# Optimization experiments

Hardware: AMD Instinct MI355X
Metric: run time of the kernel (lower is better)

## Reference

```python
import jax, jax.numpy as jnp
import numpy as np

QI8 = 127.0      # qint8 symmetric max
QI16 = 32767.0   # qint16 symmetric max
MIN_SUB_OUT = -12.0  # SegmentLUT exp input_range lower bound
EPS = 1e-9


def _fq(x, scale, qmax):
    # fake-quantize with straight-through estimator
    q = jnp.clip(jnp.round(x / scale), -qmax - 1.0, qmax) * scale
    return x + jax.lax.stop_gradient(q - x)


def _fq_auto(x, qmax):
    # symmetric max-abs observer (scale is not differentiated, as in QAT)
    s = jax.lax.stop_gradient(jnp.maximum(jnp.max(jnp.abs(x)), EPS)) / qmax
    return _fq(x, s, qmax)


def setup_inputs() -> dict:
    key = jax.random.key(0)
    # pre-softmax logits, quantized with scale 0.0625 -> int8 range ~[-8, 8]
    x = jax.random.normal(key, (8, 4096, 1024), dtype=jnp.float32) * 2.0
    scale = jnp.ones((1,), dtype=jnp.float32) * 0.0625
    return {"x": x, "scale": scale}


def reference(x, scale):
    dim = 1
    # input fake-quant to qint8 grid with given scale (QuantiSoftmaxFunction.forward)
    xq = _fq(x, scale, QI8)
    # sub: x - max(x, dim), qint16 fake-quant (FloatFunctional.sub with int16 qconfig)
    sub = xq - jnp.max(xq, axis=dim, keepdims=True)  # values in (-inf, 0]
    # SegmentLUT exp: input clipped to [min_sub_out, 0], zero gradient below range
    sub = _fq_auto(jnp.clip(sub, MIN_SUB_OUT, 0.0), QI16)
    e = _fq_auto(jnp.exp(sub), QI16)               # LUT exp, qint16 out
    s = _fq_auto(jnp.sum(e, axis=dim, keepdims=True), QI16)  # qint16 sum
    r = _fq_auto(1.0 / s, QI16)                    # LUT reciprocal, qint16
    out = _fq_auto(e * r, QI8)                     # final mul, qint8 output
    return out
```

## Files before the change

kernel.cpp:

```cpp
#include <hip/hip_runtime.h>
#include <math.h>


typedef float       f4 __attribute__((ext_vector_type(4)));
typedef signed char c4 __attribute__((ext_vector_type(4)));

static constexpr int Bdim = 8;
static constexpr int Jdim = 4096;
static constexpr int Cdim = 1024;
static constexpr int JCHUNK = 16;
static constexpr int NJC = Jdim / JCHUNK;
static constexpr int NG = Bdim * Cdim;
static constexpr int PSIZE = Bdim * NJC * Cdim;

static constexpr int SC_OFF   = 0;
static constexpr int GMAX_OFF = 16;
static constexpr int S_OFF    = GMAX_OFF + NG;
static constexpr int PS_OFF   = S_OFF + NG;
static constexpr size_t FB_FLOATS   = (size_t)PS_OFF + PSIZE;
static constexpr size_t FB_BYTES    = FB_FLOATS * 4;
static constexpr size_t CODES_BYTES = (size_t)Bdim * Jdim * Cdim;
static constexpr size_t P_BYTES     = 2 * (size_t)PSIZE;

__device__ __forceinline__ float code8(float x, float sinv) {
    return fminf(fmaxf(rintf(x * sinv), -128.0f), 127.0f);
}

__device__ __forceinline__ float eq_from(float xq, float gmv, float ssub_inv, float ssub) {
    float sub = fminf(fmaxf(xq - gmv, -12.0f), 0.0f);
    float q   = rintf(sub * ssub_inv);
    float e   = __expf(q * ssub);
    return rintf(e * 32767.0f) * (1.0f / 32767.0f);
}

template <bool WC>
__global__ __launch_bounds__(256) void k_pass1(const float* __restrict__ x,
                                               const float* __restrict__ scale,
                                               float* __restrict__ fbuf,
                                               signed char* __restrict__ codes,
                                               signed char* __restrict__ pmax,
                                               signed char* __restrict__ pmin) {
    if (blockIdx.x == 0 && threadIdx.x == 0) {
        fbuf[SC_OFF + 0] = 0.0f;
        fbuf[SC_OFF + 1] = 0.0f;
        fbuf[SC_OFF + 2] = __int_as_float(0x7f800000);
    }
    const int b  = blockIdx.x / NJC;
    const int jc = blockIdx.x % NJC;
    const int c0 = threadIdx.x * 4;
    const float sinv = 1.0f / scale[0];
    const size_t base = ((size_t)(b * Jdim + jc * JCHUNK)) * Cdim + c0;

    f4 vmax = {-1e30f, -1e30f, -1e30f, -1e30f};
    f4 vmin = { 1e30f,  1e30f,  1e30f,  1e30f};
    #pragma unroll 4
    for (int r = 0; r < JCHUNK; ++r) {
        const f4 v = __builtin_nontemporal_load(
            reinterpret_cast<const f4*>(x + base + (size_t)r * Cdim));
        f4 q;
        q[0] = code8(v[0], sinv); q[1] = code8(v[1], sinv);
        q[2] = code8(v[2], sinv); q[3] = code8(v[3], sinv);
        vmax[0] = fmaxf(vmax[0], q[0]); vmin[0] = fminf(vmin[0], q[0]);
        vmax[1] = fmaxf(vmax[1], q[1]); vmin[1] = fminf(vmin[1], q[1]);
        vmax[2] = fmaxf(vmax[2], q[2]); vmin[2] = fminf(vmin[2], q[2]);
        vmax[3] = fmaxf(vmax[3], q[3]); vmin[3] = fminf(vmin[3], q[3]);
        if (WC) {
            c4 pk = {(signed char)(int)q[0], (signed char)(int)q[1],
                     (signed char)(int)q[2], (signed char)(int)q[3]};
            *reinterpret_cast<c4*>(codes + base + (size_t)r * Cdim) = pk;
        }
    }
    const size_t pidx = ((size_t)(b * NJC + jc)) * Cdim + c0;
    c4 mx = {(signed char)(int)vmax[0], (signed char)(int)vmax[1],
             (signed char)(int)vmax[2], (signed char)(int)vmax[3]};
    c4 mn = {(signed char)(int)vmin[0], (signed char)(int)vmin[1],
             (signed char)(int)vmin[2], (signed char)(int)vmin[3]};
    *reinterpret_cast<c4*>(pmax + pidx) = mx;
    *reinterpret_cast<c4*>(pmin + pidx) = mn;
}

__global__ __launch_bounds__(256) void k_reduce1(const float* __restrict__ scale,
                                                 float* __restrict__ fbuf,
                                                 const signed char* __restrict__ pmax,
                                                 const signed char* __restrict__ pmin) {
    const int b   = blockIdx.x / 32;
    const int ct  = blockIdx.x % 32;
    const int ci  = threadIdx.x & 31;
    const int sub = threadIdx.x >> 5;
    const int c   = ct * 32 + ci;

    int mx = -128, mn = 127;
    for (int jc = sub; jc < NJC; jc += 8) {
        const size_t idx = ((size_t)(b * NJC + jc)) * Cdim + c;
        mx = max(mx, (int)pmax[idx]);
        mn = min(mn, (int)pmin[idx]);
    }
    __shared__ int smx[8][32], smn[8][32];
    smx[sub][ci] = mx; smn[sub][ci] = mn;
    __syncthreads();
    for (int off = 4; off; off >>= 1) {
        if (sub < off) {
            smx[sub][ci] = max(smx[sub][ci], smx[sub + off][ci]);
            smn[sub][ci] = min(smn[sub][ci], smn[sub + off][ci]);
        }
        __syncthreads();
    }
    __shared__ float sd[32];
    if (sub == 0) {
        const float s = scale[0];
        const float gmaxv = (float)smx[0][ci] * s;
        const float gminv = (float)smn[0][ci] * s;
        fbuf[GMAX_OFF + b * Cdim + c] = (float)smx[0][ci];
        sd[ci] = fminf(12.0f, gmaxv - gminv);
    }
    __syncthreads();
    if (threadIdx.x == 0) {
        float m = sd[0];
        #pragma unroll
        for (int i = 1; i < 32; ++i) m = fmaxf(m, sd[i]);
        atomicMax(reinterpret_cast<unsigned int*>(fbuf + SC_OFF + 0), __float_as_uint(m));
    }
}

template <bool UC>
__global__ __launch_bounds__(256) void k_pass2(const float* __restrict__ x,
                                               const signed char* __restrict__ codes,
                                               const float* __restrict__ scale,
                                               float* __restrict__ fbuf) {
    const int b  = blockIdx.x / NJC;
    const int jc = blockIdx.x % NJC;
    const int c0 = threadIdx.x * 4;
    const float s = scale[0];
    const float sinv = 1.0f / s;
    const float amax = fmaxf(fbuf[SC_OFF + 0], 1e-9f);
    const float ssub = amax / 32767.0f;
    const float ssub_inv = 1.0f / ssub;
    const f4 gmc = *reinterpret_cast<const f4*>(fbuf + GMAX_OFF + b * Cdim + c0);
    const float gm0 = gmc[0] * s, gm1 = gmc[1] * s, gm2 = gmc[2] * s, gm3 = gmc[3] * s;
    const size_t base = ((size_t)(b * Jdim + jc * JCHUNK)) * Cdim + c0;

    float a0 = 0.f, a1 = 0.f, a2 = 0.f, a3 = 0.f;
    #pragma unroll 4
    for (int r = 0; r < JCHUNK; ++r) {
        float xq0, xq1, xq2, xq3;
        if (UC) {
            const c4 q = *reinterpret_cast<const c4*>(codes + base + (size_t)r * Cdim);
            xq0 = (float)q[0] * s; xq1 = (float)q[1] * s;
            xq2 = (float)q[2] * s; xq3 = (float)q[3] * s;
        } else {
            const f4 v = *reinterpret_cast<const f4*>(x + base + (size_t)r * Cdim);
            xq0 = code8(v[0], sinv) * s; xq1 = code8(v[1], sinv) * s;
            xq2 = code8(v[2], sinv) * s; xq3 = code8(v[3], sinv) * s;
        }
        a0 += eq_from(xq0, gm0, ssub_inv, ssub);
        a1 += eq_from(xq1, gm1, ssub_inv, ssub);
        a2 += eq_from(xq2, gm2, ssub_inv, ssub);
        a3 += eq_from(xq3, gm3, ssub_inv, ssub);
    }
    f4 acc = {a0, a1, a2, a3};
    *reinterpret_cast<f4*>(fbuf + PS_OFF + ((size_t)(b * NJC + jc)) * Cdim + c0) = acc;
}

__global__ __launch_bounds__(256) void k_reduce2(float* __restrict__ fbuf) {
    const int b   = blockIdx.x / 32;
    const int ct  = blockIdx.x % 32;
    const int ci  = threadIdx.x & 31;
    const int sub = threadIdx.x >> 5;
    const int c   = ct * 32 + ci;

    float p = 0.0f;
    for (int jc = sub; jc < NJC; jc += 8)
        p += fbuf[PS_OFF + ((size_t)(b * NJC + jc)) * Cdim + c];
    __shared__ float sp[8][32];
    sp[sub][ci] = p;
    __syncthreads();
    for (int off = 4; off; off >>= 1) {
        if (sub < off) sp[sub][ci] += sp[sub + off][ci];
        __syncthreads();
    }
    __shared__ float smx[32], smn[32];
    if (sub == 0) {
        const float t = sp[0][ci];
        fbuf[S_OFF + b * Cdim + c] = t;
        smx[ci] = t; smn[ci] = t;
    }
    __syncthreads();
    if (threadIdx.x == 0) {
        float mx = smx[0], mn = smn[0];
        #pragma unroll
        for (int i = 1; i < 32; ++i) { mx = fmaxf(mx, smx[i]); mn = fminf(mn, smn[i]); }
        atomicMax(reinterpret_cast<unsigned int*>(fbuf + SC_OFF + 1), __float_as_uint(mx));
        atomicMin(reinterpret_cast<unsigned int*>(fbuf + SC_OFF + 2), __float_as_uint(mn));
    }
}

template <bool UC>
__global__ __launch_bounds__(256) void k_pass3(const float* __restrict__ x,
                                               const signed char* __restrict__ codes,
                                               const float* __restrict__ scale,
                                               const float* __restrict__ fbuf,
                                               float* __restrict__ out) {
    const int b  = blockIdx.x / NJC;
    const int jc = blockIdx.x % NJC;
    const int c0 = threadIdx.x * 4;
    const float s = scale[0];
    const float sinv = 1.0f / s;

    const float amax = fmaxf(fbuf[SC_OFF + 0], 1e-9f);
    const float ssub = amax / 32767.0f;
    const float ssub_inv = 1.0f / ssub;

    const float max_s = fbuf[SC_OFF + 1];
    const float min_s = fbuf[SC_OFF + 2];
    const float scale_s = fmaxf(max_s, 1e-9f) / 32767.0f;
    const float ss_inv = 1.0f / scale_s;
    const float minsq = fminf(fmaxf(rintf(min_s * ss_inv), -32768.0f), 32767.0f) * scale_s;
    const float maxr  = 1.0f / minsq;
    const float scale_r = fmaxf(maxr, 1e-9f) / 32767.0f;
    const float sr_inv  = 1.0f / scale_r;
    const float maxrq = fminf(fmaxf(rintf(maxr * sr_inv), -32768.0f), 32767.0f) * scale_r;
    const float scale_out = fmaxf(maxrq, 1e-9f) / 127.0f;
    const float so_inv = 1.0f / scale_out;

    const f4 gmc = *reinterpret_cast<const f4*>(fbuf + GMAX_OFF + b * Cdim + c0);
    const float gm0 = gmc[0] * s, gm1 = gmc[1] * s, gm2 = gmc[2] * s, gm3 = gmc[3] * s;
    const f4 s4 = *reinterpret_cast<const f4*>(fbuf + S_OFF + b * Cdim + c0);

    f4 rq;
    {
        float q0 = fminf(fmaxf(rintf(s4[0] * ss_inv), -32768.0f), 32767.0f) * scale_s;
        float q1 = fminf(fmaxf(rintf(s4[1] * ss_inv), -32768.0f), 32767.0f) * scale_s;
        float q2 = fminf(fmaxf(rintf(s4[2] * ss_inv), -32768.0f), 32767.0f) * scale_s;
        float q3 = fminf(fmaxf(rintf(s4[3] * ss_inv), -32768.0f), 32767.0f) * scale_s;
        rq[0] = fminf(fmaxf(rintf((1.0f / q0) * sr_inv), -32768.0f), 32767.0f) * scale_r;
        rq[1] = fminf(fmaxf(rintf((1.0f / q1) * sr_inv), -32768.0f), 32767.0f) * scale_r;
        rq[2] = fminf(fmaxf(rintf((1.0f / q2) * sr_inv), -32768.0f), 32767.0f) * scale_r;
        rq[3] = fminf(fmaxf(rintf((1.0f / q3) * sr_inv), -32768.0f), 32767.0f) * scale_r;
    }

    const size_t base = ((size_t)(b * Jdim + jc * JCHUNK)) * Cdim + c0;
    #pragma unroll 4
    for (int r = 0; r < JCHUNK; ++r) {
        float xq0, xq1, xq2, xq3;
        if (UC) {
            const c4 q = *reinterpret_cast<const c4*>(codes + base + (size_t)r * Cdim);
            xq0 = (float)q[0] * s; xq1 = (float)q[1] * s;
            xq2 = (float)q[2] * s; xq3 = (float)q[3] * s;
        } else {
            const f4 v = *reinterpret_cast<const f4*>(x + base + (size_t)r * Cdim);
            xq0 = code8(v[0], sinv) * s; xq1 = code8(v[1], sinv) * s;
            xq2 = code8(v[2], sinv) * s; xq3 = code8(v[3], sinv) * s;
        }
        float e0 = eq_from(xq0, gm0, ssub_inv, ssub) * rq[0];
        float e1 = eq_from(xq1, gm1, ssub_inv, ssub) * rq[1];
        float e2 = eq_from(xq2, gm2, ssub_inv, ssub) * rq[2];
        float e3 = eq_from(xq3, gm3, ssub_inv, ssub) * rq[3];
        f4 o;
        o[0] = fminf(fmaxf(rintf(e0 * so_inv), -128.0f), 127.0f) * scale_out;
        o[1] = fminf(fmaxf(rintf(e1 * so_inv), -128.0f), 127.0f) * scale_out;
        o[2] = fminf(fmaxf(rintf(e2 * so_inv), -128.0f), 127.0f) * scale_out;
        o[3] = fminf(fmaxf(rintf(e3 * so_inv), -128.0f), 127.0f) * scale_out;
        __builtin_nontemporal_store(o, reinterpret_cast<f4*>(out + base + (size_t)r * Cdim));
    }
}

extern "C" void kernel_launch(void* const* d_in, const int* in_sizes, int n_in,
                              void* d_out, int out_size, void* d_ws, size_t ws_size,
                              hipStream_t stream) {
    const float* x     = (const float*)d_in[0];
    const float* scale = (const float*)d_in[1];
    float* out = (float*)d_out;

    const bool uc = ws_size >= CODES_BYTES + FB_BYTES + P_BYTES;
    signed char* codes = uc ? (signed char*)d_ws : nullptr;
    float* fbuf = uc ? (float*)((char*)d_ws + CODES_BYTES) : (float*)d_ws;
    signed char* pmax = (signed char*)((char*)fbuf + FB_BYTES);
    signed char* pmin = pmax + PSIZE;

    if (uc) {
        k_pass1<true ><<<Bdim * NJC, 256, 0, stream>>>(x, scale, fbuf, codes, pmax, pmin);
        k_reduce1<<<256, 256, 0, stream>>>(scale, fbuf, pmax, pmin);
        k_pass2<true ><<<Bdim * NJC, 256, 0, stream>>>(x, codes, scale, fbuf);
        k_reduce2<<<256, 256, 0, stream>>>(fbuf);
        k_pass3<true ><<<Bdim * NJC, 256, 0, stream>>>(x, codes, scale, fbuf, out);
    } else {
        k_pass1<false><<<Bdim * NJC, 256, 0, stream>>>(x, scale, fbuf, codes, pmax, pmin);
        k_reduce1<<<256, 256, 0, stream>>>(scale, fbuf, pmax, pmin);
        k_pass2<false><<<Bdim * NJC, 256, 0, stream>>>(x, codes, scale, fbuf);
        k_reduce2<<<256, 256, 0, stream>>>(fbuf);
        k_pass3<false><<<Bdim * NJC, 256, 0, stream>>>(x, codes, scale, fbuf, out);
    }
}
```

Before: 101.4 us.

## Fuse five-kernel softmax pipeline into one cooperative kernel with register-resident codes

Replaces the pass1/reduce1/pass2/reduce2/pass3 chain with a single cooperative kernel of 256 blocks by 1024 threads. Each thread keeps its 32 int8 codes in registers, and grid-wide syncs handle the two global scalar reductions. This removes the intermediate codes and partial buffers in global memory, the repeated reads of those codes, and four extra launches. The cost is two grid barriers and high register pressure at 1024 threads per block; the old path runs only if the cooperative launch fails.

```diff
diff --git a/kernel.cpp b/kernel.cpp
--- a/kernel.cpp
+++ b/kernel.cpp
@@ -1,5 +1,8 @@
 #include <hip/hip_runtime.h>
+#include <hip/hip_cooperative_groups.h>
 #include <math.h>
+
+namespace cgx = cooperative_groups;
 
 
 typedef float       f4 __attribute__((ext_vector_type(4)));
@@ -8,30 +11,218 @@
 static constexpr int Bdim = 8;
 static constexpr int Jdim = 4096;
 static constexpr int Cdim = 1024;
-static constexpr int JCHUNK = 16;
-static constexpr int NJC = Jdim / JCHUNK;
-static constexpr int NG = Bdim * Cdim;
-static constexpr int PSIZE = Bdim * NJC * Cdim;
-
-static constexpr int SC_OFF   = 0;
-static constexpr int GMAX_OFF = 16;
-static constexpr int S_OFF    = GMAX_OFF + NG;
-static constexpr int PS_OFF   = S_OFF + NG;
-static constexpr size_t FB_FLOATS   = (size_t)PS_OFF + PSIZE;
-static constexpr size_t FB_BYTES    = FB_FLOATS * 4;
-static constexpr size_t CODES_BYTES = (size_t)Bdim * Jdim * Cdim;
-static constexpr size_t P_BYTES     = 2 * (size_t)PSIZE;
-
-__device__ __forceinline__ float code8(float x, float sinv) {
+
+static constexpr int CT    = 32;
+static constexpr int NCT   = Cdim / CT;
+static constexpr int FGRID = Bdim * NCT;
+static constexpr int FBLK  = 1024;
+static constexpr int KROWS = 32;
+static constexpr int RSTEP = 128;
+
+__device__ __forceinline__ float code8f(float x, float sinv) {
     return fminf(fmaxf(rintf(x * sinv), -128.0f), 127.0f);
 }
-
 __device__ __forceinline__ float eq_from(float xq, float gmv, float ssub_inv, float ssub) {
     float sub = fminf(fmaxf(xq - gmv, -12.0f), 0.0f);
     float q   = rintf(sub * ssub_inv);
     float e   = __expf(q * ssub);
     return rintf(e * 32767.0f) * (1.0f / 32767.0f);
 }
+
+__device__ __forceinline__ f4 shfl_xor4(f4 v, int off) {
+    f4 r; r[0] = __shfl_xor(v[0], off); r[1] = __shfl_xor(v[1], off);
+    r[2] = __shfl_xor(v[2], off); r[3] = __shfl_xor(v[3], off); return r;
+}
+__device__ __forceinline__ f4 fmax4v(f4 a, f4 b) {
+    f4 r; r[0]=fmaxf(a[0],b[0]); r[1]=fmaxf(a[1],b[1]);
+    r[2]=fmaxf(a[2],b[2]); r[3]=fmaxf(a[3],b[3]); return r;
+}
+__device__ __forceinline__ f4 fmin4v(f4 a, f4 b) {
+    f4 r; r[0]=fminf(a[0],b[0]); r[1]=fminf(a[1],b[1]);
+    r[2]=fminf(a[2],b[2]); r[3]=fminf(a[3],b[3]); return r;
+}
+__device__ __forceinline__ f4 add4v(f4 a, f4 b) {
+    f4 r; r[0]=a[0]+b[0]; r[1]=a[1]+b[1]; r[2]=a[2]+b[2]; r[3]=a[3]+b[3]; return r;
+}
+
+__global__ __launch_bounds__(FBLK, 4) void k_fused(const float* __restrict__ x,
+                                                   const float* __restrict__ scale,
+                                                   float* __restrict__ out,
+                                                   float* __restrict__ wsf) {
+    const int bid   = blockIdx.x;
+    const int b     = bid / NCT;
+    const int ctile = bid % NCT;
+    const int t     = threadIdx.x;
+    const int cgp   = t & 7;
+    const int rg    = t >> 3;
+    const int w     = t >> 6;
+    const int l     = t & 63;
+    const float s    = scale[0];
+    const float sinv = 1.0f / s;
+
+    float* dblk  = wsf;
+    float* smaxb = wsf + 256;
+    float* sminb = wsf + 512;
+
+    __shared__ f4 lA[16][8], lB[16][8];
+    __shared__ f4 gmaxs[8];
+    __shared__ f4 scol[8];
+    __shared__ float bc[3];
+
+    const size_t base = ((size_t)b * Jdim + rg) * Cdim + (size_t)(ctile * CT + cgp * 4);
+
+    c4 codes[KROWS];
+    f4 vmax = {-1e30f, -1e30f, -1e30f, -1e30f};
+    f4 vmin = { 1e30f,  1e30f,  1e30f,  1e30f};
+#pragma unroll
+    for (int k = 0; k < KROWS; ++k) {
+        const f4 v = __builtin_nontemporal_load(
+            reinterpret_cast<const f4*>(x + base + (size_t)k * RSTEP * Cdim));
+        f4 q;
+        q[0] = code8f(v[0], sinv); q[1] = code8f(v[1], sinv);
+        q[2] = code8f(v[2], sinv); q[3] = code8f(v[3], sinv);
+        vmax = fmax4v(vmax, q); vmin = fmin4v(vmin, q);
+        codes[k] = (c4){(signed char)(int)q[0], (signed char)(int)q[1],
+                        (signed char)(int)q[2], (signed char)(int)q[3]};
+    }
+#pragma unroll
+    for (int off = 8; off < 64; off <<= 1) {
+        vmax = fmax4v(vmax, shfl_xor4(vmax, off));
+        vmin = fmin4v(vmin, shfl_xor4(vmin, off));
+    }
+    if (l < 8) { lA[w][l] = vmax; lB[w][l] = vmin; }
+    __syncthreads();
+    if (w == 0) {
+        const int wcg = l & 7, wi = l >> 3;
+        f4 m = fmax4v(lA[wi][wcg], lA[wi + 8][wcg]);
+        f4 n = fmin4v(lB[wi][wcg], lB[wi + 8][wcg]);
+#pragma unroll
+        for (int off = 8; off < 64; off <<= 1) {
+            m = fmax4v(m, shfl_xor4(m, off));
+            n = fmin4v(n, shfl_xor4(n, off));
+        }
+        if (l < 8) gmaxs[l] = m;
+        float d;
+        {
+            float d0 = fminf(12.0f, m[0]*s - n[0]*s);
+            float d1 = fminf(12.0f, m[1]*s - n[1]*s);
+            float d2 = fminf(12.0f, m[2]*s - n[2]*s);
+            float d3 = fminf(12.0f, m[3]*s - n[3]*s);
+            d = fmaxf(fmaxf(d0, d1), fmaxf(d2, d3));
+        }
+#pragma unroll
+        for (int off = 1; off < 8; off <<= 1) d = fmaxf(d, __shfl_xor(d, off));
+        if (l == 0) dblk[bid] = d;
+    }
+    cgx::this_grid().sync();
+
+    if (w == 0) {
+        const f4 dv = *reinterpret_cast<const f4*>(dblk + 4 * l);
+        float dm = fmaxf(fmaxf(dv[0], dv[1]), fmaxf(dv[2], dv[3]));
+#pragma unroll
+        for (int off = 1; off < 64; off <<= 1) dm = fmaxf(dm, __shfl_xor(dm, off));
+        if (l == 0) bc[0] = dm;
+    }
+    __syncthreads();
+    const float amax = fmaxf(bc[0], 1e-9f);
+    const float ssub = amax / 32767.0f;
+    const float ssub_inv = 1.0f / ssub;
+    const f4 gmc = gmaxs[cgp];
+    const f4 gm  = {gmc[0]*s, gmc[1]*s, gmc[2]*s, gmc[3]*s};
+
+    f4 acc = {0.f, 0.f, 0.f, 0.f};
+#pragma unroll
+    for (int k = 0; k < KROWS; ++k) {
+        const c4 q = codes[k];
+        acc[0] += eq_from((float)q[0]*s, gm[0], ssub_inv, ssub);
+        acc[1] += eq_from((float)q[1]*s, gm[1], ssub_inv, ssub);
+        acc[2] += eq_from((float)q[2]*s, gm[2], ssub_inv, ssub);
+        acc[3] += eq_from((float)q[3]*s, gm[3], ssub_inv, ssub);
+    }
+#pragma unroll
+    for (int off = 8; off < 64; off <<= 1) acc = add4v(acc, shfl_xor4(acc, off));
+    if (l < 8) lA[w][l] = acc;
+    __syncthreads();
+    if (w == 0) {
+        const int wcg = l & 7, wi = l >> 3;
+        f4 tsum = add4v(lA[wi][wcg], lA[wi + 8][wcg]);
+#pragma unroll
+        for (int off = 8; off < 64; off <<= 1) tsum = add4v(tsum, shfl_xor4(tsum, off));
+        if (l < 8) scol[l] = tsum;
+        float mx = fmaxf(fmaxf(tsum[0], tsum[1]), fmaxf(tsum[2], tsum[3]));
+        float mn = fminf(fminf(tsum[0], tsum[1]), fminf(tsum[2], tsum[3]));
+#pragma unroll
+        for (int off = 1; off < 8; off <<= 1) {
+            mx = fmaxf(mx, __shfl_xor(mx, off));
+            mn = fminf(mn, __shfl_xor(mn, off));
+        }
+        if (l == 0) { smaxb[bid] = mx; sminb[bid] = mn; }
+    }
+    cgx::this_grid().sync();
+
+    if (w == 0) {
+        const f4 mv = *reinterpret_cast<const f4*>(smaxb + 4 * l);
+        const f4 nv = *reinterpret_cast<const f4*>(sminb + 4 * l);
+        float mx = fmaxf(fmaxf(mv[0], mv[1]), fmaxf(mv[2], mv[3]));
+        float mn = fminf(fminf(nv[0], nv[1]), fminf(nv[2], nv[3]));
+#pragma unroll
+        for (int off = 1; off < 64; off <<= 1) {
+            mx = fmaxf(mx, __shfl_xor(mx, off));
+            mn = fminf(mn, __shfl_xor(mn, off));
+        }
+        if (l == 0) { bc[1] = mx; bc[2] = mn; }
+    }
+    __syncthreads();
+    const float max_s = bc[1], min_s = bc[2];
+    const float scale_s = fmaxf(max_s, 1e-9f) / 32767.0f;
+    const float ss_inv  = 1.0f / scale_s;
+    const float minsq   = fminf(fmaxf(rintf(min_s * ss_inv), -32768.0f), 32767.0f) * scale_s;
+    const float maxr    = 1.0f / minsq;
+    const float scale_r = fmaxf(maxr, 1e-9f) / 32767.0f;
+    const float sr_inv  = 1.0f / scale_r;
+    const float maxrq   = fminf(fmaxf(rintf(maxr * sr_inv), -32768.0f), 32767.0f) * scale_r;
+    const float scale_out = fmaxf(maxrq, 1e-9f) / 127.0f;
+    const float so_inv  = 1.0f / scale_out;
+
+    const f4 sc = scol[cgp];
+    f4 rq;
+#pragma unroll
+    for (int i = 0; i < 4; ++i) {
+        float qv = fminf(fmaxf(rintf(sc[i] * ss_inv), -32768.0f), 32767.0f) * scale_s;
+        rq[i] = fminf(fmaxf(rintf((1.0f / qv) * sr_inv), -32768.0f), 32767.0f) * scale_r;
+    }
+
+#pragma unroll
+    for (int k = 0; k < KROWS; ++k) {
+        const c4 q = codes[k];
+        f4 o;
+        {
+            float e0 = eq_from((float)q[0]*s, gm[0], ssub_inv, ssub) * rq[0];
+            float e1 = eq_from((float)q[1]*s, gm[1], ssub_inv, ssub) * rq[1];
+            float e2 = eq_from((float)q[2]*s, gm[2], ssub_inv, ssub) * rq[2];
+            float e3 = eq_from((float)q[3]*s, gm[3], ssub_inv, ssub) * rq[3];
+            o[0] = fminf(fmaxf(rintf(e0 * so_inv), -128.0f), 127.0f) * scale_out;
+            o[1] = fminf(fmaxf(rintf(e1 * so_inv), -128.0f), 127.0f) * scale_out;
+            o[2] = fminf(fmaxf(rintf(e2 * so_inv), -128.0f), 127.0f) * scale_out;
+            o[3] = fminf(fmaxf(rintf(e3 * so_inv), -128.0f), 127.0f) * scale_out;
+        }
+        __builtin_nontemporal_store(o,
+            reinterpret_cast<f4*>(out + base + (size_t)k * RSTEP * Cdim));
+    }
+}
+
+static constexpr int JCHUNK = 16;
+static constexpr int NJC = Jdim / JCHUNK;
+static constexpr int NG = Bdim * Cdim;
+static constexpr int PSIZE = Bdim * NJC * Cdim;
+
+static constexpr int SC_OFF   = 0;
+static constexpr int GMAX_OFF = 16;
+static constexpr int S_OFF    = GMAX_OFF + NG;
+static constexpr int PS_OFF   = S_OFF + NG;
+static constexpr size_t FB_BYTES    = ((size_t)PS_OFF + PSIZE) * 4;
+static constexpr size_t CODES_BYTES = (size_t)Bdim * Jdim * Cdim;
+static constexpr size_t P_BYTES     = 2 * (size_t)PSIZE;
 
 template <bool WC>
 __global__ __launch_bounds__(256) void k_pass1(const float* __restrict__ x,
@@ -58,12 +249,9 @@
         const f4 v = __builtin_nontemporal_load(
             reinterpret_cast<const f4*>(x + base + (size_t)r * Cdim));
         f4 q;
-        q[0] = code8(v[0], sinv); q[1] = code8(v[1], sinv);
-        q[2] = code8(v[2], sinv); q[3] = code8(v[3], sinv);
-        vmax[0] = fmaxf(vmax[0], q[0]); vmin[0] = fminf(vmin[0], q[0]);
-        vmax[1] = fmaxf(vmax[1], q[1]); vmin[1] = fminf(vmin[1], q[1]);
-        vmax[2] = fmaxf(vmax[2], q[2]); vmin[2] = fminf(vmin[2], q[2]);
-        vmax[3] = fmaxf(vmax[3], q[3]); vmin[3] = fminf(vmin[3], q[3]);
+        q[0] = code8f(v[0], sinv); q[1] = code8f(v[1], sinv);
+        q[2] = code8f(v[2], sinv); q[3] = code8f(v[3], sinv);
+        vmax = fmax4v(vmax, q); vmin = fmin4v(vmin, q);
         if (WC) {
             c4 pk = {(signed char)(int)q[0], (signed char)(int)q[1],
                      (signed char)(int)q[2], (signed char)(int)q[3]};
@@ -108,10 +296,8 @@
     __shared__ float sd[32];
     if (sub == 0) {
         const float s = scale[0];
-        const float gmaxv = (float)smx[0][ci] * s;
-        const float gminv = (float)smn[0][ci] * s;
         fbuf[GMAX_OFF + b * Cdim + c] = (float)smx[0][ci];
-        sd[ci] = fminf(12.0f, gmaxv - gminv);
+        sd[ci] = fminf(12.0f, (float)smx[0][ci] * s - (float)smn[0][ci] * s);
     }
     __syncthreads();
     if (threadIdx.x == 0) {
@@ -136,7 +322,7 @@
     const float ssub = amax / 32767.0f;
     const float ssub_inv = 1.0f / ssub;
     const f4 gmc = *reinterpret_cast<const f4*>(fbuf + GMAX_OFF + b * Cdim + c0);
-    const float gm0 = gmc[0] * s, gm1 = gmc[1] * s, gm2 = gmc[2] * s, gm3 = gmc[3] * s;
+    const float gm0 = gmc[0]*s, gm1 = gmc[1]*s, gm2 = gmc[2]*s, gm3 = gmc[3]*s;
     const size_t base = ((size_t)(b * Jdim + jc * JCHUNK)) * Cdim + c0;
 
     float a0 = 0.f, a1 = 0.f, a2 = 0.f, a3 = 0.f;
@@ -145,12 +331,11 @@
         float xq0, xq1, xq2, xq3;
         if (UC) {
             const c4 q = *reinterpret_cast<const c4*>(codes + base + (size_t)r * Cdim);
-            xq0 = (float)q[0] * s; xq1 = (float)q[1] * s;
-            xq2 = (float)q[2] * s; xq3 = (float)q[3] * s;
+            xq0 = (float)q[0]*s; xq1 = (float)q[1]*s; xq2 = (float)q[2]*s; xq3 = (float)q[3]*s;
         } else {
             const f4 v = *reinterpret_cast<const f4*>(x + base + (size_t)r * Cdim);
-            xq0 = code8(v[0], sinv) * s; xq1 = code8(v[1], sinv) * s;
-            xq2 = code8(v[2], sinv) * s; xq3 = code8(v[3], sinv) * s;
+            xq0 = code8f(v[0], sinv)*s; xq1 = code8f(v[1], sinv)*s;
+            xq2 = code8f(v[2], sinv)*s; xq3 = code8f(v[3], sinv)*s;
         }
         a0 += eq_from(xq0, gm0, ssub_inv, ssub);
         a1 += eq_from(xq1, gm1, ssub_inv, ssub);
@@ -223,7 +408,7 @@
     const float so_inv = 1.0f / scale_out;
 
     const f4 gmc = *reinterpret_cast<const f4*>(fbuf + GMAX_OFF + b * Cdim + c0);
-    const float gm0 = gmc[0] * s, gm1 = gmc[1] * s, gm2 = gmc[2] * s, gm3 = gmc[3] * s;
+    const float gm0 = gmc[0]*s, gm1 = gmc[1]*s, gm2 = gmc[2]*s, gm3 = gmc[3]*s;
     const f4 s4 = *reinterpret_cast<const f4*>(fbuf + S_OFF + b * Cdim + c0);
 
     f4 rq;
@@ -232,10 +417,10 @@
         float q1 = fminf(fmaxf(rintf(s4[1] * ss_inv), -32768.0f), 32767.0f) * scale_s;
         float q2 = fminf(fmaxf(rintf(s4[2] * ss_inv), -32768.0f), 32767.0f) * scale_s;
         float q3 = fminf(fmaxf(rintf(s4[3] * ss_inv), -32768.0f), 32767.0f) * scale_s;
-        rq[0] = fminf(fmaxf(rintf((1.0f / q0) * sr_inv), -32768.0f), 32767.0f) * scale_r;
-        rq[1] = fminf(fmaxf(rintf((1.0f / q1) * sr_inv), -32768.0f), 32767.0f) * scale_r;
-        rq[2] = fminf(fmaxf(rintf((1.0f / q2) * sr_inv), -32768.0f), 32767.0f) * scale_r;
-        rq[3] = fminf(fmaxf(rintf((1.0f / q3) * sr_inv), -32768.0f), 32767.0f) * scale_r;
+        rq[0] = fminf(fmaxf(rintf((1.0f/q0) * sr_inv), -32768.0f), 32767.0f) * scale_r;
+        rq[1] = fminf(fmaxf(rintf((1.0f/q1) * sr_inv), -32768.0f), 32767.0f) * scale_r;
+        rq[2] = fminf(fmaxf(rintf((1.0f/q2) * sr_inv), -32768.0f), 32767.0f) * scale_r;
+        rq[3] = fminf(fmaxf(rintf((1.0f/q3) * sr_inv), -32768.0f), 32767.0f) * scale_r;
     }
 
     const size_t base = ((size_t)(b * Jdim + jc * JCHUNK)) * Cdim + c0;
@@ -244,12 +429,11 @@
         float xq0, xq1, xq2, xq3;
         if (UC) {
             const c4 q = *reinterpret_cast<const c4*>(codes + base + (size_t)r * Cdim);
-            xq0 = (float)q[0] * s; xq1 = (float)q[1] * s;
-            xq2 = (float)q[2] * s; xq3 = (float)q[3] * s;
+            xq0 = (float)q[0]*s; xq1 = (float)q[1]*s; xq2 = (float)q[2]*s; xq3 = (float)q[3]*s;
         } else {
             const f4 v = *reinterpret_cast<const f4*>(x + base + (size_t)r * Cdim);
-            xq0 = code8(v[0], sinv) * s; xq1 = code8(v[1], sinv) * s;
-            xq2 = code8(v[2], sinv) * s; xq3 = code8(v[3], sinv) * s;
+            xq0 = code8f(v[0], sinv)*s; xq1 = code8f(v[1], sinv)*s;
+            xq2 = code8f(v[2], sinv)*s; xq3 = code8f(v[3], sinv)*s;
         }
         float e0 = eq_from(xq0, gm0, ssub_inv, ssub) * rq[0];
         float e1 = eq_from(xq1, gm1, ssub_inv, ssub) * rq[1];
@@ -270,6 +454,16 @@
     const float* x     = (const float*)d_in[0];
     const float* scale = (const float*)d_in[1];
     float* out = (float*)d_out;
+
+    {
+        float* wsf = (float*)d_ws;
+        const float* xa = x; const float* sa = scale; float* oa = out; float* wa = wsf;
+        void* args[4] = {(void*)&xa, (void*)&sa, (void*)&oa, (void*)&wa};
+        hipError_t err = hipLaunchCooperativeKernel((const void*)k_fused,
+                                                    dim3(FGRID), dim3(FBLK),
+                                                    args, 0, stream);
+        if (err == hipSuccess) return;
+    }
 
     const bool uc = ws_size >= CODES_BYTES + FB_BYTES + P_BYTES;
     signed char* codes = uc ? (signed char*)d_ws : nullptr;
```

After: 188.4 us. +85.7%, slower.

## Fuse column-sum reduction into pass2 and drop separate reduce kernel

Applied to the files above, without the earlier changes.

Pass 2 is reorganized so each block owns 16 columns across the full sequence dimension and reduces the exp sums in-block with shuffles and shared memory, writing final sums and atomically updating global min/max. This removes the partial-sum buffer and the reduce2 launch. Pass 1 and pass 3 batch eight row loads before computing, and partial max/min arrays are transposed for coalesced reduction. The new pass-2 access pattern reads narrow 16-byte segments per row, which may reduce memory efficiency.

```diff
diff --git a/kernel.cpp b/kernel.cpp
--- a/kernel.cpp
+++ b/kernel.cpp
@@ -8,92 +8,109 @@
 static constexpr int Bdim = 8;
 static constexpr int Jdim = 4096;
 static constexpr int Cdim = 1024;
-static constexpr int JCHUNK = 16;
-static constexpr int NJC = Jdim / JCHUNK;
-static constexpr int NG = Bdim * Cdim;
-static constexpr int PSIZE = Bdim * NJC * Cdim;
-
-static constexpr int SC_OFF   = 0;
-static constexpr int GMAX_OFF = 16;
-static constexpr int S_OFF    = GMAX_OFF + NG;
-static constexpr int PS_OFF   = S_OFF + NG;
-static constexpr size_t FB_FLOATS   = (size_t)PS_OFF + PSIZE;
-static constexpr size_t FB_BYTES    = FB_FLOATS * 4;
-static constexpr size_t CODES_BYTES = (size_t)Bdim * Jdim * Cdim;
-static constexpr size_t P_BYTES     = 2 * (size_t)PSIZE;
-
-__device__ __forceinline__ float code8(float x, float sinv) {
+static constexpr int NG   = Bdim * Cdim;
+
+static constexpr int JC1   = 16;
+static constexpr int NJC   = Jdim / JC1;
+static constexpr int GRID1 = Bdim * NJC;
+
+static constexpr size_t SC_B    = 0;
+static constexpr size_t GMV_B   = 1024;
+static constexpr size_t SARR_B  = 36864;
+static constexpr size_t PMAX_B  = 131072;
+static constexpr size_t PMIN_B  = PMAX_B + 2097152;
+static constexpr size_t CODES_B = 8388608;
+static constexpr size_t WS_FULL = CODES_B + 33554432;
+static constexpr size_t WS_MIN  = PMIN_B + 2097152;
+
+__device__ __forceinline__ float code8f(float x, float sinv) {
     return fminf(fmaxf(rintf(x * sinv), -128.0f), 127.0f);
 }
-
 __device__ __forceinline__ float eq_from(float xq, float gmv, float ssub_inv, float ssub) {
     float sub = fminf(fmaxf(xq - gmv, -12.0f), 0.0f);
     float q   = rintf(sub * ssub_inv);
     float e   = __expf(q * ssub);
     return rintf(e * 32767.0f) * (1.0f / 32767.0f);
 }
+__device__ __forceinline__ f4 shfl_xor4(f4 v, int off) {
+    f4 r; r[0] = __shfl_xor(v[0], off); r[1] = __shfl_xor(v[1], off);
+    r[2] = __shfl_xor(v[2], off); r[3] = __shfl_xor(v[3], off); return r;
+}
+__device__ __forceinline__ f4 fmax4v(f4 a, f4 b) {
+    f4 r; r[0]=fmaxf(a[0],b[0]); r[1]=fmaxf(a[1],b[1]);
+    r[2]=fmaxf(a[2],b[2]); r[3]=fmaxf(a[3],b[3]); return r;
+}
+__device__ __forceinline__ f4 fmin4v(f4 a, f4 b) {
+    f4 r; r[0]=fminf(a[0],b[0]); r[1]=fminf(a[1],b[1]);
+    r[2]=fminf(a[2],b[2]); r[3]=fminf(a[3],b[3]); return r;
+}
+__device__ __forceinline__ f4 add4v(f4 a, f4 b) {
+    f4 r; r[0]=a[0]+b[0]; r[1]=a[1]+b[1]; r[2]=a[2]+b[2]; r[3]=a[3]+b[3]; return r;
+}
 
 template <bool WC>
-__global__ __launch_bounds__(256) void k_pass1(const float* __restrict__ x,
-                                               const float* __restrict__ scale,
-                                               float* __restrict__ fbuf,
-                                               signed char* __restrict__ codes,
-                                               signed char* __restrict__ pmax,
-                                               signed char* __restrict__ pmin) {
+__global__ __launch_bounds__(256) void k_p1(const float* __restrict__ x,
+                                            const float* __restrict__ scale,
+                                            char* __restrict__ ws) {
+    float* sc = (float*)(ws + SC_B);
     if (blockIdx.x == 0 && threadIdx.x == 0) {
-        fbuf[SC_OFF + 0] = 0.0f;
-        fbuf[SC_OFF + 1] = 0.0f;
-        fbuf[SC_OFF + 2] = __int_as_float(0x7f800000);
+        sc[0] = 0.0f;
+        sc[1] = 0.0f;
+        sc[2] = __int_as_float(0x7f800000);
     }
     const int b  = blockIdx.x / NJC;
     const int jc = blockIdx.x % NJC;
     const int c0 = threadIdx.x * 4;
     const float sinv = 1.0f / scale[0];
-    const size_t base = ((size_t)(b * Jdim + jc * JCHUNK)) * Cdim + c0;
+    const size_t base = ((size_t)(b * Jdim + jc * JC1)) * Cdim + c0;
+    signed char* codes = (signed char*)(ws + CODES_B);
 
     f4 vmax = {-1e30f, -1e30f, -1e30f, -1e30f};
     f4 vmin = { 1e30f,  1e30f,  1e30f,  1e30f};
-    #pragma unroll 4
-    for (int r = 0; r < JCHUNK; ++r) {
-        const f4 v = __builtin_nontemporal_load(
-            reinterpret_cast<const f4*>(x + base + (size_t)r * Cdim));
-        f4 q;
-        q[0] = code8(v[0], sinv); q[1] = code8(v[1], sinv);
-        q[2] = code8(v[2], sinv); q[3] = code8(v[3], sinv);
-        vmax[0] = fmaxf(vmax[0], q[0]); vmin[0] = fminf(vmin[0], q[0]);
-        vmax[1] = fmaxf(vmax[1], q[1]); vmin[1] = fminf(vmin[1], q[1]);
-        vmax[2] = fmaxf(vmax[2], q[2]); vmin[2] = fminf(vmin[2], q[2]);
-        vmax[3] = fmaxf(vmax[3], q[3]); vmin[3] = fminf(vmin[3], q[3]);
-        if (WC) {
-            c4 pk = {(signed char)(int)q[0], (signed char)(int)q[1],
-                     (signed char)(int)q[2], (signed char)(int)q[3]};
-            *reinterpret_cast<c4*>(codes + base + (size_t)r * Cdim) = pk;
-        }
-    }
-    const size_t pidx = ((size_t)(b * NJC + jc)) * Cdim + c0;
-    c4 mx = {(signed char)(int)vmax[0], (signed char)(int)vmax[1],
+#pragma unroll
+    for (int r0 = 0; r0 < JC1; r0 += 8) {
+        f4 v[8];
+#pragma unroll
+        for (int j = 0; j < 8; ++j)
+            v[j] = __builtin_nontemporal_load(
+                reinterpret_cast<const f4*>(x + base + (size_t)(r0 + j) * Cdim));
+#pragma unroll
+        for (int j = 0; j < 8; ++j) {
+            f4 q;
+            q[0] = code8f(v[j][0], sinv); q[1] = code8f(v[j][1], sinv);
+            q[2] = code8f(v[j][2], sinv); q[3] = code8f(v[j][3], sinv);
+            vmax = fmax4v(vmax, q); vmin = fmin4v(vmin, q);
+            if (WC)
+                *reinterpret_cast<c4*>(codes + base + (size_t)(r0 + j) * Cdim) =
+                    (c4){(signed char)(int)q[0], (signed char)(int)q[1],
+                         (signed char)(int)q[2], (signed char)(int)q[3]};
+        }
+    }
+    const size_t pidx = (size_t)jc * NG + b * Cdim + c0;
+    *reinterpret_cast<c4*>(ws + PMAX_B + pidx) =
+        (c4){(signed char)(int)vmax[0], (signed char)(int)vmax[1],
              (signed char)(int)vmax[2], (signed char)(int)vmax[3]};
-    c4 mn = {(signed char)(int)vmin[0], (signed char)(int)vmin[1],
+    *reinterpret_cast<c4*>(ws + PMIN_B + pidx) =
+        (c4){(signed char)(int)vmin[0], (signed char)(int)vmin[1],
              (signed char)(int)vmin[2], (signed char)(int)vmin[3]};
-    *reinterpret_cast<c4*>(pmax + pidx) = mx;
-    *reinterpret_cast<c4*>(pmin + pidx) = mn;
-}
-
-__global__ __launch_bounds__(256) void k_reduce1(const float* __restrict__ scale,
-                                                 float* __restrict__ fbuf,
-                                                 const signed char* __restrict__ pmax,
-                                                 const signed char* __restrict__ pmin) {
-    const int b   = blockIdx.x / 32;
-    const int ct  = blockIdx.x % 32;
+}
+
+__global__ __launch_bounds__(256) void k_r1(const float* __restrict__ scale,
+                                            char* __restrict__ ws) {
+    const signed char* pmax8 = (const signed char*)(ws + PMAX_B);
+    const signed char* pmin8 = (const signed char*)(ws + PMIN_B);
+    float* gmv = (float*)(ws + GMV_B);
+    float* sc  = (float*)(ws + SC_B);
+
     const int ci  = threadIdx.x & 31;
     const int sub = threadIdx.x >> 5;
-    const int c   = ct * 32 + ci;
+    const int g   = blockIdx.x * 32 + ci;
 
     int mx = -128, mn = 127;
     for (int jc = sub; jc < NJC; jc += 8) {
-        const size_t idx = ((size_t)(b * NJC + jc)) * Cdim + c;
-        mx = max(mx, (int)pmax[idx]);
-        mn = min(mn, (int)pmin[idx]);
+        const size_t idx = (size_t)jc * NG + g;
+        mx = max(mx, (int)pmax8[idx]);
+        mn = min(mn, (int)pmin8[idx]);
     }
     __shared__ int smx[8][32], smn[8][32];
     smx[sub][ci] = mx; smn[sub][ci] = mn;
@@ -108,159 +125,168 @@
     __shared__ float sd[32];
     if (sub == 0) {
         const float s = scale[0];
-        const float gmaxv = (float)smx[0][ci] * s;
-        const float gminv = (float)smn[0][ci] * s;
-        fbuf[GMAX_OFF + b * Cdim + c] = (float)smx[0][ci];
-        sd[ci] = fminf(12.0f, gmaxv - gminv);
+        gmv[g] = (float)smx[0][ci];
+        sd[ci] = fminf(12.0f, (float)smx[0][ci] * s - (float)smn[0][ci] * s);
     }
     __syncthreads();
     if (threadIdx.x == 0) {
         float m = sd[0];
-        #pragma unroll
+#pragma unroll
         for (int i = 1; i < 32; ++i) m = fmaxf(m, sd[i]);
-        atomicMax(reinterpret_cast<unsigned int*>(fbuf + SC_OFF + 0), __float_as_uint(m));
+        atomicMax(reinterpret_cast<unsigned int*>(sc + 0), __float_as_uint(m));
     }
 }
 
 template <bool UC>
-__global__ __launch_bounds__(256) void k_pass2(const float* __restrict__ x,
-                                               const signed char* __restrict__ codes,
-                                               const float* __restrict__ scale,
-                                               float* __restrict__ fbuf) {
+__global__ __launch_bounds__(512) void k_p2(const float* __restrict__ x,
+                                            const float* __restrict__ scale,
+                                            char* __restrict__ ws) {
+    const int g0 = blockIdx.x * 16;
+    const int b  = g0 >> 10;
+    const int cb = g0 & 1023;
+    const int t  = threadIdx.x;
+    const int cq = t & 3;
+    const int rs = t >> 2;
+    const int w  = t >> 6;
+    const int l  = t & 63;
+
+    const float s = scale[0];
+    const float sinv = 1.0f / s;
+    float* sc   = (float*)(ws + SC_B);
+    float* gmv  = (float*)(ws + GMV_B);
+    float* sarr = (float*)(ws + SARR_B);
+    const signed char* codes = (const signed char*)(ws + CODES_B);
+
+    const float amax = fmaxf(sc[0], 1e-9f);
+    const float ssub = amax / 32767.0f;
+    const float ssub_inv = 1.0f / ssub;
+    const f4 gmc = *reinterpret_cast<const f4*>(gmv + g0 + cq * 4);
+    const f4 gm  = {gmc[0] * s, gmc[1] * s, gmc[2] * s, gmc[3] * s};
+
+    const size_t base = ((size_t)(b * Jdim + rs)) * Cdim + (size_t)(cb + cq * 4);
+
+    f4 acc = {0.f, 0.f, 0.f, 0.f};
+#pragma unroll 8
+    for (int k = 0; k < 32; ++k) {
+        float xq0, xq1, xq2, xq3;
+        if (UC) {
+            const c4 q = *reinterpret_cast<const c4*>(codes + base + (size_t)k * 128 * Cdim);
+            xq0 = (float)q[0] * s; xq1 = (float)q[1] * s;
+            xq2 = (float)q[2] * s; xq3 = (float)q[3] * s;
+        } else {
+            const f4 v = *reinterpret_cast<const f4*>(x + base + (size_t)k * 128 * Cdim);
+            xq0 = code8f(v[0], sinv) * s; xq1 = code8f(v[1], sinv) * s;
+            xq2 = code8f(v[2], sinv) * s; xq3 = code8f(v[3], sinv) * s;
+        }
+        acc[0] += eq_from(xq0, gm[0], ssub_inv, ssub);
+        acc[1] += eq_from(xq1, gm[1], ssub_inv, ssub);
+        acc[2] += eq_from(xq2, gm[2], ssub_inv, ssub);
+        acc[3] += eq_from(xq3, gm[3], ssub_inv, ssub);
+    }
+#pragma unroll
+    for (int off = 4; off < 64; off <<= 1) acc = add4v(acc, shfl_xor4(acc, off));
+
+    __shared__ f4 lA[8][4];
+    __shared__ float smx8[8], smn8[8];
+    if (l < 4) lA[w][l] = acc;
+    __syncthreads();
+    if (w == 0 && l < 32) {
+        const int wi = l >> 2, cg = l & 3;
+        f4 tsum = lA[wi][cg];
+#pragma unroll
+        for (int off = 4; off < 32; off <<= 1) tsum = add4v(tsum, shfl_xor4(tsum, off));
+        if (l < 4) {
+            *reinterpret_cast<f4*>(sarr + g0 + l * 4) = tsum;
+            float mx = fmaxf(fmaxf(tsum[0], tsum[1]), fmaxf(tsum[2], tsum[3]));
+            float mn = fminf(fminf(tsum[0], tsum[1]), fminf(tsum[2], tsum[3]));
+            mx = fmaxf(mx, __shfl_xor(mx, 1)); mn = fminf(mn, __shfl_xor(mn, 1));
+            mx = fmaxf(mx, __shfl_xor(mx, 2)); mn = fminf(mn, __shfl_xor(mn, 2));
+            if (l == 0) { smx8[0] = mx; smn8[0] = mn; }
+        }
+    }
+    __syncthreads();
+    if (t == 0) {
+        atomicMax(reinterpret_cast<unsigned int*>(sc + 1), __float_as_uint(smx8[0]));
+        atomicMin(reinterpret_cast<unsigned int*>(sc + 2), __float_as_uint(smn8[0]));
+    }
+}
+
+template <bool UC>
+__global__ __launch_bounds__(256) void k_p3(const float* __restrict__ x,
+                                            const float* __restrict__ scale,
+                                            const char* __restrict__ ws,
+                                            float* __restrict__ out) {
     const int b  = blockIdx.x / NJC;
     const int jc = blockIdx.x % NJC;
     const int c0 = threadIdx.x * 4;
     const float s = scale[0];
     const float sinv = 1.0f / s;
-    const float amax = fmaxf(fbuf[SC_OFF + 0], 1e-9f);
+    const float* sc   = (const float*)(ws + SC_B);
+    const float* gmv  = (const float*)(ws + GMV_B);
+    const float* sarr = (const float*)(ws + SARR_B);
+    const signed char* codes = (const signed char*)(ws + CODES_B);
+
+    const float amax = fmaxf(sc[0], 1e-9f);
     const float ssub = amax / 32767.0f;
     const float ssub_inv = 1.0f / ssub;
-    const f4 gmc = *reinterpret_cast<const f4*>(fbuf + GMAX_OFF + b * Cdim + c0);
-    const float gm0 = gmc[0] * s, gm1 = gmc[1] * s, gm2 = gmc[2] * s, gm3 = gmc[3] * s;
-    const size_t base = ((size_t)(b * Jdim + jc * JCHUNK)) * Cdim + c0;
-
-    float a0 = 0.f, a1 = 0.f, a2 = 0.f, a3 = 0.f;
-    #pragma unroll 4
-    for (int r = 0; r < JCHUNK; ++r) {
-        float xq0, xq1, xq2, xq3;
-        if (UC) {
-            const c4 q = *reinterpret_cast<const c4*>(codes + base + (size_t)r * Cdim);
-            xq0 = (float)q[0] * s; xq1 = (float)q[1] * s;
-            xq2 = (float)q[2] * s; xq3 = (float)q[3] * s;
-        } else {
-            const f4 v = *reinterpret_cast<const f4*>(x + base + (size_t)r * Cdim);
-            xq0 = code8(v[0], sinv) * s; xq1 = code8(v[1], sinv) * s;
-            xq2 = code8(v[2], sinv) * s; xq3 = code8(v[3], sinv) * s;
-        }
-        a0 += eq_from(xq0, gm0, ssub_inv, ssub);
-        a1 += eq_from(xq1, gm1, ssub_inv, ssub);
-        a2 += eq_from(xq2, gm2, ssub_inv, ssub);
-        a3 += eq_from(xq3, gm3, ssub_inv, ssub);
-    }
-    f4 acc = {a0, a1, a2, a3};
-    *reinterpret_cast<f4*>(fbuf + PS_OFF + ((size_t)(b * NJC + jc)) * Cdim + c0) = acc;
-}
-
-__global__ __launch_bounds__(256) void k_reduce2(float* __restrict__ fbuf) {
-    const int b   = blockIdx.x / 32;
-    const int ct  = blockIdx.x % 32;
-    const int ci  = threadIdx.x & 31;
-    const int sub = threadIdx.x >> 5;
-    const int c   = ct * 32 + ci;
-
-    float p = 0.0f;
-    for (int jc = sub; jc < NJC; jc += 8)
-        p += fbuf[PS_OFF + ((size_t)(b * NJC + jc)) * Cdim + c];
-    __shared__ float sp[8][32];
-    sp[sub][ci] = p;
-    __syncthreads();
-    for (int off = 4; off; off >>= 1) {
-        if (sub < off) sp[sub][ci] += sp[sub + off][ci];
-        __syncthreads();
-    }
-    __shared__ float smx[32], smn[32];
-    if (sub == 0) {
-        const float t = sp[0][ci];
-        fbuf[S_OFF + b * Cdim + c] = t;
-        smx[ci] = t; smn[ci] = t;
-    }
-    __syncthreads();
-    if (threadIdx.x == 0) {
-        float mx = smx[0], mn = smn[0];
-        #pragma unroll
-        for (int i = 1; i < 32; ++i) { mx = fmaxf(mx, smx[i]); mn = fminf(mn, smn[i]); }
-        atomicMax(reinterpret_cast<unsigned int*>(fbuf + SC_OFF + 1), __float_as_uint(mx));
-        atomicMin(reinterpret_cast<unsigned int*>(fbuf + SC_OFF + 2), __float_as_uint(mn));
-    }
-}
-
-template <bool UC>
-__global__ __launch_bounds__(256) void k_pass3(const float* __restrict__ x,
-                                               const signed char* __restrict__ codes,
-                                               const float* __restrict__ scale,
-                                               const float* __restrict__ fbuf,
-                                               float* __restrict__ out) {
-    const int b  = blockIdx.x / NJC;
-    const int jc = blockIdx.x % NJC;
-    const int c0 = threadIdx.x * 4;
-    const float s = scale[0];
-    const float sinv = 1.0f / s;
-
-    const float amax = fmaxf(fbuf[SC_OFF + 0], 1e-9f);
-    const float ssub = amax / 32767.0f;
-    const float ssub_inv = 1.0f / ssub;
-
-    const float max_s = fbuf[SC_OFF + 1];
-    const float min_s = fbuf[SC_OFF + 2];
+
+    const float max_s = sc[1];
+    const float min_s = sc[2];
     const float scale_s = fmaxf(max_s, 1e-9f) / 32767.0f;
-    const float ss_inv = 1.0f / scale_s;
-    const float minsq = fminf(fmaxf(rintf(min_s * ss_inv), -32768.0f), 32767.0f) * scale_s;
-    const float maxr  = 1.0f / minsq;
+    const float ss_inv  = 1.0f / scale_s;
+    const float minsq   = fminf(fmaxf(rintf(min_s * ss_inv), -32768.0f), 32767.0f) * scale_s;
+    const float maxr    = 1.0f / minsq;
     const float scale_r = fmaxf(maxr, 1e-9f) / 32767.0f;
     const float sr_inv  = 1.0f / scale_r;
-    const float maxrq = fminf(fmaxf(rintf(maxr * sr_inv), -32768.0f), 32767.0f) * scale_r;
+    const float maxrq   = fminf(fmaxf(rintf(maxr * sr_inv), -32768.0f), 32767.0f) * scale_r;
     const float scale_out = fmaxf(maxrq, 1e-9f) / 127.0f;
-    const float so_inv = 1.0f / scale_out;
-
-    const f4 gmc = *reinterpret_cast<const f4*>(fbuf + GMAX_OFF + b * Cdim + c0);
-    const float gm0 = gmc[0] * s, gm1 = gmc[1] * s, gm2 = gmc[2] * s, gm3 = gmc[3] * s;
-    const f4 s4 = *reinterpret_cast<const f4*>(fbuf + S_OFF + b * Cdim + c0);
+    const float so_inv  = 1.0f / scale_out;
+
+    const f4 gmc = *reinterpret_cast<const f4*>(gmv + b * Cdim + c0);
+    const f4 gm  = {gmc[0] * s, gmc[1] * s, gmc[2] * s, gmc[3] * s};
+    const f4 s4  = *reinterpret_cast<const f4*>(sarr + b * Cdim + c0);
 
     f4 rq;
-    {
-        float q0 = fminf(fmaxf(rintf(s4[0] * ss_inv), -32768.0f), 32767.0f) * scale_s;
-        float q1 = fminf(fmaxf(rintf(s4[1] * ss_inv), -32768.0f), 32767.0f) * scale_s;
-        float q2 = fminf(fmaxf(rintf(s4[2] * ss_inv), -32768.0f), 32767.0f) * scale_s;
-        float q3 = fminf(fmaxf(rintf(s4[3] * ss_inv), -32768.0f), 32767.0f) * scale_s;
-        rq[0] = fminf(fmaxf(rintf((1.0f / q0) * sr_inv), -32768.0f), 32767.0f) * scale_r;
-        rq[1] = fminf(fmaxf(rintf((1.0f / q1) * sr_inv), -32768.0f), 32767.0f) * scale_r;
-        rq[2] = fminf(fmaxf(rintf((1.0f / q2) * sr_inv), -32768.0f), 32767.0f) * scale_r;
-        rq[3] = fminf(fmaxf(rintf((1.0f / q3) * sr_inv), -32768.0f), 32767.0f) * scale_r;
-    }
-
-    const size_t base = ((size_t)(b * Jdim + jc * JCHUNK)) * Cdim + c0;
-    #pragma unroll 4
-    for (int r = 0; r < JCHUNK; ++r) {
-        float xq0, xq1, xq2, xq3;
-        if (UC) {
-            const c4 q = *reinterpret_cast<const c4*>(codes + base + (size_t)r * Cdim);
-            xq0 = (float)q[0] * s; xq1 = (float)q[1] * s;
-            xq2 = (float)q[2] * s; xq3 = (float)q[3] * s;
-        } else {
-            const f4 v = *reinterpret_cast<const f4*>(x + base + (size_t)r * Cdim);
-            xq0 = code8(v[0], sinv) * s; xq1 = code8(v[1], sinv) * s;
-            xq2 = code8(v[2], sinv) * s; xq3 = code8(v[3], sinv) * s;
-        }
-        float e0 = eq_from(xq0, gm0, ssub_inv, ssub) * rq[0];
-        float e1 = eq_from(xq1, gm1, ssub_inv, ssub) * rq[1];
-        float e2 = eq_from(xq2, gm2, ssub_inv, ssub) * rq[2];
-        float e3 = eq_from(xq3, gm3, ssub_inv, ssub) * rq[3];
-        f4 o;
-        o[0] = fminf(fmaxf(rintf(e0 * so_inv), -128.0f), 127.0f) * scale_out;
-        o[1] = fminf(fmaxf(rintf(e1 * so_inv), -128.0f), 127.0f) * scale_out;
-        o[2] = fminf(fmaxf(rintf(e2 * so_inv), -128.0f), 127.0f) * scale_out;
-        o[3] = fminf(fmaxf(rintf(e3 * so_inv), -128.0f), 127.0f) * scale_out;
-        __builtin_nontemporal_store(o, reinterpret_cast<f4*>(out + base + (size_t)r * Cdim));
+#pragma unroll
+    for (int i = 0; i < 4; ++i) {
+        float qv = fminf(fmaxf(rintf(s4[i] * ss_inv), -32768.0f), 32767.0f) * scale_s;
+        rq[i] = fminf(fmaxf(rintf((1.0f / qv) * sr_inv), -32768.0f), 32767.0f) * scale_r;
+    }
+
+    const size_t base = ((size_t)(b * Jdim + jc * JC1)) * Cdim + c0;
+#pragma unroll
+    for (int r0 = 0; r0 < JC1; r0 += 8) {
+        c4 qv[8];
+        f4 xv[8];
+#pragma unroll
+        for (int j = 0; j < 8; ++j) {
+            if (UC)
+                qv[j] = *reinterpret_cast<const c4*>(codes + base + (size_t)(r0 + j) * Cdim);
+            else
+                xv[j] = *reinterpret_cast<const f4*>(x + base + (size_t)(r0 + j) * Cdim);
+        }
+#pragma unroll
+        for (int j = 0; j < 8; ++j) {
+            float xq0, xq1, xq2, xq3;
+            if (UC) {
+                xq0 = (float)qv[j][0] * s; xq1 = (float)qv[j][1] * s;
+                xq2 = (float)qv[j][2] * s; xq3 = (float)qv[j][3] * s;
+            } else {
+                xq0 = code8f(xv[j][0], sinv) * s; xq1 = code8f(xv[j][1], sinv) * s;
+                xq2 = code8f(xv[j][2], sinv) * s; xq3 = code8f(xv[j][3], sinv) * s;
+            }
+            const float e0 = eq_from(xq0, gm[0], ssub_inv, ssub) * rq[0];
+            const float e1 = eq_from(xq1, gm[1], ssub_inv, ssub) * rq[1];
+            const float e2 = eq_from(xq2, gm[2], ssub_inv, ssub) * rq[2];
+            const float e3 = eq_from(xq3, gm[3], ssub_inv, ssub) * rq[3];
+            f4 o;
+            o[0] = fminf(fmaxf(rintf(e0 * so_inv), -128.0f), 127.0f) * scale_out;
+            o[1] = fminf(fmaxf(rintf(e1 * so_inv), -128.0f), 127.0f) * scale_out;
+            o[2] = fminf(fmaxf(rintf(e2 * so_inv), -128.0f), 127.0f) * scale_out;
+            o[3] = fminf(fmaxf(rintf(e3 * so_inv), -128.0f), 127.0f) * scale_out;
+            __builtin_nontemporal_store(o,
+                reinterpret_cast<f4*>(out + base + (size_t)(r0 + j) * Cdim));
+        }
     }
 }
 
@@ -270,24 +296,17 @@
     const float* x     = (const float*)d_in[0];
     const float* scale = (const float*)d_in[1];
     float* out = (float*)d_out;
-
-    const bool uc = ws_size >= CODES_BYTES + FB_BYTES + P_BYTES;
-    signed char* codes = uc ? (signed char*)d_ws : nullptr;
-    float* fbuf = uc ? (float*)((char*)d_ws + CODES_BYTES) : (float*)d_ws;
-    signed char* pmax = (signed char*)((char*)fbuf + FB_BYTES);
-    signed char* pmin = pmax + PSIZE;
-
-    if (uc) {
-        k_pass1<true ><<<Bdim * NJC, 256, 0, stream>>>(x, scale, fbuf, codes, pmax, pmin);
-        k_reduce1<<<256, 256, 0, stream>>>(scale, fbuf, pmax, pmin);
-        k_pass2<true ><<<Bdim * NJC, 256, 0, stream>>>(x, codes, scale, fbuf);
-        k_reduce2<<<256, 256, 0, stream>>>(fbuf);
-        k_pass3<true ><<<Bdim * NJC, 256, 0, stream>>>(x, codes, scale, fbuf, out);
+    char* ws   = (char*)d_ws;
+
+    if (ws_size >= WS_FULL) {
+        k_p1<true ><<<GRID1, 256, 0, stream>>>(x, scale, ws);
+        k_r1<<<NG / 32, 256, 0, stream>>>(scale, ws);
+        k_p2<true ><<<NG / 16, 512, 0, stream>>>(x, scale, ws);
+        k_p3<true ><<<GRID1, 256, 0, stream>>>(x, scale, ws, out);
     } else {
-        k_pass1<false><<<Bdim * NJC, 256, 0, stream>>>(x, scale, fbuf, codes, pmax, pmin);
-        k_reduce1<<<256, 256, 0, stream>>>(scale, fbuf, pmax, pmin);
-        k_pass2<false><<<Bdim * NJC, 256, 0, stream>>>(x, codes, scale, fbuf);
-        k_reduce2<<<256, 256, 0, stream>>>(fbuf);
-        k_pass3<false><<<Bdim * NJC, 256, 0, stream>>>(x, codes, scale, fbuf, out);
-    }
-}
+        k_p1<false><<<GRID1, 256, 0, stream>>>(x, scale, ws);
+        k_r1<<<NG / 32, 256, 0, stream>>>(scale, ws);
+        k_p2<false><<<NG / 16, 512, 0, stream>>>(x, scale, ws);
+        k_p3<false><<<GRID1, 256, 0, stream>>>(x, scale, ws, out);
+    }
+}
```

Measured after the change: 112.7 us. +11.1%, slower.
